# Kernel optimization log

Measured on AMD Instinct MI355X. Metric: run time of the kernel, lower is better.

## Reference

```python
import jax, jax.numpy as jnp
import numpy as np

B, L, V = 16, 2048, 64


def setup_inputs() -> dict:
    key = jax.random.key(0)
    k1, k2, k3, k4 = jax.random.split(key, 4)
    idx = jax.random.randint(k1, (B, L), 0, V)                      # tokens
    Wq_w = jax.random.normal(k2, (V, V), jnp.float32) * 0.02         # nn.Linear weight
    Wv_w = jax.random.normal(k3, (V, V), jnp.float32) * 0.02 + np.float32(np.e)  # Wv.weight (+e init)
    v_emb = jax.random.normal(k4, (L, 1), jnp.float32) * 0.02        # nn.Embedding(length, 1)
    return {"idx": idx, "Wq_w": Wq_w, "Wv_w": Wv_w, "v_emb": v_emb}


def reference(idx, Wq_w, Wv_w, v_emb):
    Lx = v_emb.shape[0]
    Vx = Wq_w.shape[0]
    # e = one_hot token embedding, [B, L, V]
    e = jax.nn.one_hot(idx, Vx, dtype=jnp.float32)
    i = jnp.arange(Lx)
    # pos[i, j] = max(i - j, 0); learned relative-position score table [L, L]
    pos = jnp.maximum(i[:, None] - i[None, :], 0)
    pos_embd = v_emb[pos, 0]
    causal = i[:, None] >= i[None, :]                                # tril mask
    # Attention block 1: scores are the learned position table (no QK^T)
    attn1 = jax.nn.softmax(jnp.where(causal, pos_embd, -jnp.inf), axis=-1)  # [L, L]
    l1 = jnp.einsum('ts,bsv->btv', attn1, e)                         # [B, L, V]
    # Attention block 2: Wq(e) @ l1^T, masked softmax, attn @ e * scalar
    q = jnp.einsum('btv,uv->btu', e, Wq_w)                           # F.linear: e @ Wq^T
    scores = jnp.einsum('btv,bsv->bts', q, l1)                       # [B, L, L]
    attn2 = jax.nn.softmax(jnp.where(causal, scores, -jnp.inf), axis=-1)
    l2 = jnp.einsum('bts,bsv->btv', attn2, e) * Wv_w[0, 0]           # logits [B, L, V]
    return l2
```

## Files before the change

### kernel.cpp

```cpp
#include <hip/hip_runtime.h>


#define LSEQ 2048
#define NB 16
#define NV 64
#define NC 32
#define NBLK 1024
#define BPB 64

typedef __attribute__((ext_vector_type(8))) short bf16x8;
typedef __attribute__((ext_vector_type(4))) float f32x4;

__device__ __forceinline__ unsigned short f2bf(float f) {
  unsigned int u = __float_as_uint(f);
  return (unsigned short)((u + 0x7FFFu + ((u >> 16) & 1u)) >> 16);
}

__device__ __forceinline__ void bb_arrive(unsigned int* cnt, unsigned int* flag) {
  __syncthreads();
  if (threadIdx.x == 0) {
    unsigned int old = __hip_atomic_fetch_add(cnt, 1u, __ATOMIC_RELAXED,
                                              __HIP_MEMORY_SCOPE_AGENT);
    if (old == BPB - 1u)
      __hip_atomic_store(flag, 1u, __ATOMIC_RELAXED, __HIP_MEMORY_SCOPE_AGENT);
  }
}
__device__ __forceinline__ void bb_wait(unsigned int* flag) {
  if (threadIdx.x == 0) {
    while (__hip_atomic_load(flag, __ATOMIC_RELAXED,
                             __HIP_MEMORY_SCOPE_AGENT) == 0u)
      __builtin_amdgcn_s_sleep(2);
  }
  __syncthreads();
}

__global__ __launch_bounds__(256, 4) void k_fused(
    const int* __restrict__ idx, const float* __restrict__ Wq,
    const float* __restrict__ Wv, const float* __restrict__ v_emb,
    unsigned short* __restrict__ Agr, float* __restrict__ P,
    float* __restrict__ out, unsigned int* __restrict__ bar) {
  union SMem {
    struct {
      unsigned short GL0[2208];
      unsigned short GL1[2176];
      float Sarr[2048];
      float red[16][64];
      float red2[16][64];
    } g;
    struct {
      float Hs[NC][65];
      float pl[4][64];
      unsigned long long mk[4][64];
    } s;
  };
  __shared__ SMem sm;
  __shared__ float swsum[4];

  const int bid = blockIdx.x;
  const int tid = threadIdx.x;
  const int w = tid >> 6;
  const int lane = tid & 63;
  const int b = bid >> 6;

  unsigned int* cnt0b  = bar +    0 + b * 32;
  unsigned int* flag0b = bar +  512 + b * 32;
  unsigned int* cnt1b  = bar + 1024 + b * 32;
  unsigned int* flag1b = bar + 1536 + b * 32;

  {
    const int sub = bid & 63;
    const int k8 = sub * 4 + w;
    unsigned short v[8];
#pragma unroll
    for (int j = 0; j < 8; ++j) {
      const int ii = idx[b * LSEQ + (2047 - (k8 * 8 + j))];
      v[j] = f2bf(Wq[ii * 64 + lane]);
    }
    const unsigned long long lo =
        (unsigned long long)((unsigned int)v[0] | ((unsigned int)v[1] << 16)) |
        ((unsigned long long)((unsigned int)v[2] | ((unsigned int)v[3] << 16)) << 32);
    const unsigned long long hi =
        (unsigned long long)((unsigned int)v[4] | ((unsigned int)v[5] << 16)) |
        ((unsigned long long)((unsigned int)v[6] | ((unsigned int)v[7] << 16)) << 32);
    unsigned long long* dst =
        (unsigned long long*)(Agr + ((size_t)(b * 256 + k8) * 64 + lane) * 8);
    __hip_atomic_store(dst + 0, lo, __ATOMIC_RELAXED, __HIP_MEMORY_SCOPE_AGENT);
    __hip_atomic_store(dst + 1, hi, __ATOMIC_RELAXED, __HIP_MEMORY_SCOPE_AGENT);
  }
  bb_arrive(cnt0b, flag0b);

  const int bn = 63 - (bid & 63);
  const int n0 = bn * 32;
  const int quad = lane >> 4;
  const int lm = lane & 15;
  const int nsub = w & 1;
  const int kh = w >> 1;
  const int nbase = n0 + nsub * 16;

  {
    float ev[8], ps8[8];
    float tot = 0.f;
    const int t0 = tid * 8;
#pragma unroll
    for (int j = 0; j < 8; ++j) {
      const float e = expf(v_emb[t0 + j]);
      tot += e; ev[j] = e; ps8[j] = tot;
    }
    float ws = tot;
#pragma unroll
    for (int d = 1; d < 64; d <<= 1) {
      float up = __shfl_up(ws, d);
      if (lane >= d) ws += up;
    }
    if (lane == 63) swsum[w] = ws;
    __syncthreads();
    float wbase = 0.f;
#pragma unroll
    for (int k = 0; k < 4; ++k) if (k < w) wbase += swsum[k];
    const float base = wbase + (ws - tot);
#pragma unroll
    for (int j = 0; j < 8; ++j) {
      const int d = t0 + j;
      sm.g.Sarr[d] = base + ps8[j];
      const unsigned short bv = f2bf(ev[j]);
      sm.g.GL0[d + 127] = bv;
      sm.g.GL1[d + 126] = bv;
    }
    if (tid < 31) sm.g.GL0[96 + tid] = 0;
    if (tid < 30) sm.g.GL1[96 + tid] = 0;
    if (tid == 0) { sm.g.GL0[2175] = 0; sm.g.GL1[2174] = 0; sm.g.GL1[2175] = 0; }
    __syncthreads();
  }
  const float sinv = 1.0f / sm.g.Sarr[nbase + lm];

  bb_wait(flag0b);

  {
    const unsigned long long* __restrict__ abase64 =
        (const unsigned long long*)(Agr + (size_t)b * 256 * 64 * 8);
    const int sbase = nbase + lm - 1920;
    const int kstart = 2048 - (n0 + 32);
    const int iters = bn + 1;

    f32x4 acc[4];
#pragma unroll
    for (int mt = 0; mt < 4; ++mt) acc[mt] = (f32x4){0.f, 0.f, 0.f, 0.f};

    union AF { unsigned long long q[2]; bf16x8 v; };
    union BF { unsigned int u[4]; bf16x8 v; };
    AF a[3][4];
    BF bb[3];

#define LOAD_FRAGS(J_, SL) do {                                             \
    const int k_ = kstart + (kh + 2 * (J_)) * 32;                           \
    const int kq8_ = (k_ >> 3) + quad;                                      \
    const unsigned long long* ab_ = abase64 + (size_t)(kq8_ * 64 + lm) * 2; \
    a[SL][0].q[0] = __hip_atomic_load(ab_ +  0, __ATOMIC_RELAXED, __HIP_MEMORY_SCOPE_AGENT); \
    a[SL][0].q[1] = __hip_atomic_load(ab_ +  1, __ATOMIC_RELAXED, __HIP_MEMORY_SCOPE_AGENT); \
    a[SL][1].q[0] = __hip_atomic_load(ab_ + 32, __ATOMIC_RELAXED, __HIP_MEMORY_SCOPE_AGENT); \
    a[SL][1].q[1] = __hip_atomic_load(ab_ + 33, __ATOMIC_RELAXED, __HIP_MEMORY_SCOPE_AGENT); \
    a[SL][2].q[0] = __hip_atomic_load(ab_ + 64, __ATOMIC_RELAXED, __HIP_MEMORY_SCOPE_AGENT); \
    a[SL][2].q[1] = __hip_atomic_load(ab_ + 65, __ATOMIC_RELAXED, __HIP_MEMORY_SCOPE_AGENT); \
    a[SL][3].q[0] = __hip_atomic_load(ab_ + 96, __ATOMIC_RELAXED, __HIP_MEMORY_SCOPE_AGENT); \
    a[SL][3].q[1] = __hip_atomic_load(ab_ + 97, __ATOMIC_RELAXED, __HIP_MEMORY_SCOPE_AGENT); \
    const int s_ = sbase + k_ + quad * 8;                                   \
    const unsigned int* gb_ = (s_ & 1) ? (const unsigned int*)sm.g.GL1      \
                                       : (const unsigned int*)sm.g.GL0;     \
    const int off_ = s_ >> 1;                                               \
    bb[SL].u[0] = gb_[off_ + 0]; bb[SL].u[1] = gb_[off_ + 1];               \
    bb[SL].u[2] = gb_[off_ + 2]; bb[SL].u[3] = gb_[off_ + 3];               \
  } while (0)

#define MFMA4(SL) do {                                                      \
    acc[0] = __builtin_amdgcn_mfma_f32_16x16x32_bf16(a[SL][0].v, bb[SL].v, acc[0], 0, 0, 0); \
    acc[1] = __builtin_amdgcn_mfma_f32_16x16x32_bf16(a[SL][1].v, bb[SL].v, acc[1], 0, 0, 0); \
    acc[2] = __builtin_amdgcn_mfma_f32_16x16x32_bf16(a[SL][2].v, bb[SL].v, acc[2], 0, 0, 0); \
    acc[3] = __builtin_amdgcn_mfma_f32_16x16x32_bf16(a[SL][3].v, bb[SL].v, acc[3], 0, 0, 0); \
  } while (0)

    const int J = (iters > kh) ? ((iters - kh + 1) >> 1) : 0;
    if (J > 0) {
      LOAD_FRAGS(0, 0);
      if (J > 1) LOAD_FRAGS(1, 1);
      int j = 0;
      while (true) {
        if (j + 2 < J) LOAD_FRAGS(j + 2, 2);
        MFMA4(0);
        if (++j >= J) break;
        if (j + 2 < J) LOAD_FRAGS(j + 2, 0);
        MFMA4(1);
        if (++j >= J) break;
        if (j + 2 < J) LOAD_FRAGS(j + 2, 1);
        MFMA4(2);
        if (++j >= J) break;
      }
    }
#undef LOAD_FRAGS
#undef MFMA4

    if (kh == 1) {
      float (*rd)[64] = nsub ? sm.g.red2 : sm.g.red;
#pragma unroll
      for (int mt = 0; mt < 4; ++mt)
#pragma unroll
        for (int r = 0; r < 4; ++r) rd[mt * 4 + r][lane] = acc[mt][r];
    }
    __syncthreads();
    if (kh == 0) {
      float (*rd)[64] = nsub ? sm.g.red2 : sm.g.red;
#pragma unroll
      for (int mt = 0; mt < 4; ++mt)
#pragma unroll
        for (int r = 0; r < 4; ++r) acc[mt][r] += rd[mt * 4 + r][lane];

#pragma unroll
      for (int mt = 0; mt < 4; ++mt) {
#pragma unroll
        for (int r = 0; r < 4; ++r) {
          const int c = mt * 16 + quad * 4 + r;
          const float val = __expf(acc[mt][r] * sinv);
          __hip_atomic_store(&P[((size_t)(b * 64 + c)) * LSEQ + nbase + lm],
                             val, __ATOMIC_RELAXED, __HIP_MEMORY_SCOPE_AGENT);
        }
      }
    }
  }
  bb_arrive(cnt1b, flag1b);

  {
    const int c = bid & 63;
    const int* __restrict__ irow = idx + b * LSEQ;
    int ii[8];
#pragma unroll
    for (int r = 0; r < 8; ++r)
      ii[r] = irow[(w * 8 + r) * 64 + lane];

    bb_wait(flag1b);

    const float* __restrict__ prow = P + (size_t)bid * LSEQ;
    float p[8];
#pragma unroll
    for (int r = 0; r < 8; ++r)
      p[r] = __hip_atomic_load(prow + (w * 8 + r) * 64 + lane,
                               __ATOMIC_RELAXED, __HIP_MEMORY_SCOPE_AGENT);

    for (int i = tid; i < NC * 65; i += 256) ((float*)sm.s.Hs)[i] = 0.f;
    __syncthreads();
#pragma unroll
    for (int r = 0; r < 8; ++r) atomicAdd(&sm.s.Hs[w * 8 + r][ii[r]], p[r]);
    __syncthreads();

    const int hhalf = lane >> 5, l32 = lane & 31;
#pragma unroll
    for (int r = 0; r < 8; ++r) {
      const int v = w * 16 + r * 2 + hhalf;
      const float h = sm.s.Hs[l32][v];
      float x = h;
#pragma unroll
      for (int d = 1; d < 32; d <<= 1) {
        float up = __shfl_up(x, d, 32);
        if (l32 >= d) x += up;
      }
      sm.s.Hs[l32][v] = x - h;
    }
    __syncthreads();

    const float wv = Wv[0];
#pragma unroll
    for (int r = 0; r < 8; ++r) {
      const int ch = w * 8 + r;
      unsigned long long em = __ballot(ii[r] == c);
      if (em == 0ull) continue;
      sm.s.pl[w][lane] = p[r];
      sm.s.mk[w][lane] = 0ull;
      atomicOr(&sm.s.mk[w][ii[r]], 1ull << lane);
      float ps = p[r];
#pragma unroll
      for (int d = 1; d < 64; d <<= 1) {
        float up = __shfl_up(ps, d);
        if (lane >= d) ps += up;
      }
      const float hbase = sm.s.Hs[ch][lane];
      float zex = hbase;
#pragma unroll
      for (int d = 1; d < 64; d <<= 1) zex += __shfl_xor(zex, d);
      const unsigned long long myMask = sm.s.mk[w][lane];
      while (em) {
        const int srel = __builtin_ctzll(em);
        em &= em - 1;
        unsigned long long mm = myMask &
            ((srel == 63) ? ~0ull : ((1ull << (srel + 1)) - 1ull));
        float B = hbase;
        while (mm) { const int l = __builtin_ctzll(mm); mm &= mm - 1; B += sm.s.pl[w][l]; }
        const float z = zex + __shfl(ps, srel);
        out[((size_t)(b * LSEQ + ch * 64 + srel)) * 64 + lane] = wv * B / z;
      }
    }
  }
}

extern "C" void kernel_launch(void* const* d_in, const int* in_sizes, int n_in,
                              void* d_out, int out_size, void* d_ws, size_t ws_size,
                              hipStream_t stream) {
  const int* idx     = (const int*)d_in[0];
  const float* Wq    = (const float*)d_in[1];
  const float* Wv    = (const float*)d_in[2];
  const float* v_emb = (const float*)d_in[3];
  float* out = (float*)d_out;

  float* S = (float*)d_ws;
  float* P = S + LSEQ;
  unsigned short* Ebf = (unsigned short*)(P + (size_t)NB * NV * LSEQ);
  unsigned short* Agr = Ebf + LSEQ;
  unsigned int* bar = (unsigned int*)((char*)d_ws + (16u << 20));

  hipMemsetAsync(bar, 0, 8192, stream);

  k_fused<<<dim3(NBLK), dim3(256), 0, stream>>>(idx, Wq, Wv, v_emb, Agr, P,
                                                out, bar);
}
```

Measured before the change: 123.0 us.

## Build gathered Wq fragments from LDS per block, dropping the first grid barrier

Each block now copies the whole Wq matrix (as bf16) and the reversed token-row offsets into shared memory, then assembles the MFMA A fragments by gathering from LDS. Previously a global staging buffer was written and a per-batch barrier had to complete before any block could read it. Removing the barrier and the global round trip takes away one cross-block synchronisation point and its global traffic. In exchange every block repeats the Wq load and conversion, LDS use grows (which may cut occupancy), and the scalar LDS gathers with 65-stride padding replace the vectorised global loads. The full S prefix array is also shrunk to the 32 entries each block needs.

```diff
diff --git a/kernel.cpp b/kernel.cpp
--- a/kernel.cpp
+++ b/kernel.cpp
@@ -37,15 +37,18 @@
 __global__ __launch_bounds__(256, 4) void k_fused(
     const int* __restrict__ idx, const float* __restrict__ Wq,
     const float* __restrict__ Wv, const float* __restrict__ v_emb,
-    unsigned short* __restrict__ Agr, float* __restrict__ P,
-    float* __restrict__ out, unsigned int* __restrict__ bar) {
+    float* __restrict__ P, float* __restrict__ out,
+    unsigned int* __restrict__ bar) {
   union SMem {
     struct {
+      unsigned short Wqb[64 * 65];
+      unsigned short ro[2048];
       unsigned short GL0[2208];
       unsigned short GL1[2176];
-      float Sarr[2048];
       float red[16][64];
       float red2[16][64];
+      float Spart[32];
+      float swsum[4];
     } g;
     struct {
       float Hs[NC][65];
@@ -54,7 +57,6 @@
     } s;
   };
   __shared__ SMem sm;
-  __shared__ float swsum[4];
 
   const int bid = blockIdx.x;
   const int tid = threadIdx.x;
@@ -62,32 +64,8 @@
   const int lane = tid & 63;
   const int b = bid >> 6;
 
-  unsigned int* cnt0b  = bar +    0 + b * 32;
-  unsigned int* flag0b = bar +  512 + b * 32;
-  unsigned int* cnt1b  = bar + 1024 + b * 32;
-  unsigned int* flag1b = bar + 1536 + b * 32;
-
-  {
-    const int sub = bid & 63;
-    const int k8 = sub * 4 + w;
-    unsigned short v[8];
-#pragma unroll
-    for (int j = 0; j < 8; ++j) {
-      const int ii = idx[b * LSEQ + (2047 - (k8 * 8 + j))];
-      v[j] = f2bf(Wq[ii * 64 + lane]);
-    }
-    const unsigned long long lo =
-        (unsigned long long)((unsigned int)v[0] | ((unsigned int)v[1] << 16)) |
-        ((unsigned long long)((unsigned int)v[2] | ((unsigned int)v[3] << 16)) << 32);
-    const unsigned long long hi =
-        (unsigned long long)((unsigned int)v[4] | ((unsigned int)v[5] << 16)) |
-        ((unsigned long long)((unsigned int)v[6] | ((unsigned int)v[7] << 16)) << 32);
-    unsigned long long* dst =
-        (unsigned long long*)(Agr + ((size_t)(b * 256 + k8) * 64 + lane) * 8);
-    __hip_atomic_store(dst + 0, lo, __ATOMIC_RELAXED, __HIP_MEMORY_SCOPE_AGENT);
-    __hip_atomic_store(dst + 1, hi, __ATOMIC_RELAXED, __HIP_MEMORY_SCOPE_AGENT);
-  }
-  bb_arrive(cnt0b, flag0b);
+  unsigned int* cntb  = bar +   0 + b * 32;
+  unsigned int* flagb = bar + 512 + b * 32;
 
   const int bn = 63 - (bid & 63);
   const int n0 = bn * 32;
@@ -98,6 +76,16 @@
   const int nbase = n0 + nsub * 16;
 
   {
+#pragma unroll
+    for (int u = 0; u < 16; ++u) {
+      const int e = tid * 16 + u;
+      sm.g.Wqb[(e >> 6) * 65 + (e & 63)] = f2bf(Wq[e]);
+    }
+#pragma unroll
+    for (int j = 0; j < 8; ++j) {
+      const int t = tid * 8 + j;
+      sm.g.ro[2047 - t] = (unsigned short)(idx[b * LSEQ + t] * 65);
+    }
     float ev[8], ps8[8];
     float tot = 0.f;
     const int t0 = tid * 8;
@@ -112,16 +100,17 @@
       float up = __shfl_up(ws, d);
       if (lane >= d) ws += up;
     }
-    if (lane == 63) swsum[w] = ws;
+    if (lane == 63) sm.g.swsum[w] = ws;
     __syncthreads();
     float wbase = 0.f;
 #pragma unroll
-    for (int k = 0; k < 4; ++k) if (k < w) wbase += swsum[k];
+    for (int k = 0; k < 4; ++k) if (k < w) wbase += sm.g.swsum[k];
     const float base = wbase + (ws - tot);
 #pragma unroll
     for (int j = 0; j < 8; ++j) {
       const int d = t0 + j;
-      sm.g.Sarr[d] = base + ps8[j];
+      const float Sv = base + ps8[j];
+      if ((unsigned)(d - n0) < 32u) sm.g.Spart[d - n0] = Sv;
       const unsigned short bv = f2bf(ev[j]);
       sm.g.GL0[d + 127] = bv;
       sm.g.GL1[d + 126] = bv;
@@ -131,13 +120,9 @@
     if (tid == 0) { sm.g.GL0[2175] = 0; sm.g.GL1[2174] = 0; sm.g.GL1[2175] = 0; }
     __syncthreads();
   }
-  const float sinv = 1.0f / sm.g.Sarr[nbase + lm];
-
-  bb_wait(flag0b);
+  const float sinv = 1.0f / sm.g.Spart[nsub * 16 + lm];
 
   {
-    const unsigned long long* __restrict__ abase64 =
-        (const unsigned long long*)(Agr + (size_t)b * 256 * 64 * 8);
     const int sbase = nbase + lm - 1920;
     const int kstart = 2048 - (n0 + 32);
     const int iters = bn + 1;
@@ -146,23 +131,24 @@
 #pragma unroll
     for (int mt = 0; mt < 4; ++mt) acc[mt] = (f32x4){0.f, 0.f, 0.f, 0.f};
 
-    union AF { unsigned long long q[2]; bf16x8 v; };
+    union AF { unsigned short s[8]; bf16x8 v; };
     union BF { unsigned int u[4]; bf16x8 v; };
     AF a[3][4];
     BF bb[3];
 
 #define LOAD_FRAGS(J_, SL) do {                                             \
     const int k_ = kstart + (kh + 2 * (J_)) * 32;                           \
-    const int kq8_ = (k_ >> 3) + quad;                                      \
-    const unsigned long long* ab_ = abase64 + (size_t)(kq8_ * 64 + lm) * 2; \
-    a[SL][0].q[0] = __hip_atomic_load(ab_ +  0, __ATOMIC_RELAXED, __HIP_MEMORY_SCOPE_AGENT); \
-    a[SL][0].q[1] = __hip_atomic_load(ab_ +  1, __ATOMIC_RELAXED, __HIP_MEMORY_SCOPE_AGENT); \
-    a[SL][1].q[0] = __hip_atomic_load(ab_ + 32, __ATOMIC_RELAXED, __HIP_MEMORY_SCOPE_AGENT); \
-    a[SL][1].q[1] = __hip_atomic_load(ab_ + 33, __ATOMIC_RELAXED, __HIP_MEMORY_SCOPE_AGENT); \
-    a[SL][2].q[0] = __hip_atomic_load(ab_ + 64, __ATOMIC_RELAXED, __HIP_MEMORY_SCOPE_AGENT); \
-    a[SL][2].q[1] = __hip_atomic_load(ab_ + 65, __ATOMIC_RELAXED, __HIP_MEMORY_SCOPE_AGENT); \
-    a[SL][3].q[0] = __hip_atomic_load(ab_ + 96, __ATOMIC_RELAXED, __HIP_MEMORY_SCOPE_AGENT); \
-    a[SL][3].q[1] = __hip_atomic_load(ab_ + 97, __ATOMIC_RELAXED, __HIP_MEMORY_SCOPE_AGENT); \
+    const int i0_ = k_ + quad * 8;                                          \
+    unsigned short ro_[8];                                                  \
+    *(uint4*)ro_ = *(const uint4*)&sm.g.ro[i0_];                            \
+_Pragma("unroll")                                                           \
+    for (int j_ = 0; j_ < 8; ++j_) {                                        \
+      const int base_ = (int)ro_[j_] + lm;                                  \
+      a[SL][0].s[j_] = sm.g.Wqb[base_ +  0];                                \
+      a[SL][1].s[j_] = sm.g.Wqb[base_ + 16];                                \
+      a[SL][2].s[j_] = sm.g.Wqb[base_ + 32];                                \
+      a[SL][3].s[j_] = sm.g.Wqb[base_ + 48];                                \
+    }                                                                       \
     const int s_ = sbase + k_ + quad * 8;                                   \
     const unsigned int* gb_ = (s_ & 1) ? (const unsigned int*)sm.g.GL1      \
                                        : (const unsigned int*)sm.g.GL0;     \
@@ -225,7 +211,7 @@
       }
     }
   }
-  bb_arrive(cnt1b, flag1b);
+  bb_arrive(cntb, flagb);
 
   {
     const int c = bid & 63;
@@ -235,7 +221,7 @@
     for (int r = 0; r < 8; ++r)
       ii[r] = irow[(w * 8 + r) * 64 + lane];
 
-    bb_wait(flag1b);
+    bb_wait(flagb);
 
     const float* __restrict__ prow = P + (size_t)bid * LSEQ;
     float p[8];
@@ -308,14 +294,11 @@
   const float* v_emb = (const float*)d_in[3];
   float* out = (float*)d_out;
 
-  float* S = (float*)d_ws;
-  float* P = S + LSEQ;
-  unsigned short* Ebf = (unsigned short*)(P + (size_t)NB * NV * LSEQ);
-  unsigned short* Agr = Ebf + LSEQ;
+  float* P = (float*)d_ws + LSEQ;
   unsigned int* bar = (unsigned int*)((char*)d_ws + (16u << 20));
 
   hipMemsetAsync(bar, 0, 8192, stream);
 
-  k_fused<<<dim3(NBLK), dim3(256), 0, stream>>>(idx, Wq, Wv, v_emb, Agr, P,
-                                                out, bar);
-}
+  k_fused<<<dim3(NBLK), dim3(256), 0, stream>>>(idx, Wq, Wv, v_emb, P, out,
+                                                bar);
+}
```

Result: faster. 118.5 us (-3.7%).
